# Performance work log

Hardware: AMD Instinct MI355X
Metric: run time of the kernel (lower is better)

## Reference

```python
import jax, jax.numpy as jnp
import numpy as np

EPS = 1e-12
NEG = -1e30


def setup_inputs() -> dict:
    key = jax.random.key(0)
    ks = jax.random.split(key, 7)
    B, Nq, Lp, H, D = 96, 35, 180, 768, 128
    q_hidden = jax.random.normal(ks[0], (B, Nq, H), dtype=jnp.float32)
    pos_hidden = jax.random.normal(ks[1], (B, Lp, H), dtype=jnp.float32)
    neg_hidden = jax.random.normal(ks[2], (B, Lp, H), dtype=jnp.float32)
    W = jax.random.normal(ks[3], (H, D), dtype=jnp.float32) * 0.02
    b = jax.random.normal(ks[4], (D,), dtype=jnp.float32) * 0.02
    # non-punctuation filter mask; guarantee at least one valid token per passage
    pos_mask = jax.random.bernoulli(ks[5], 0.85, (B, Lp)).at[:, 0].set(True)
    neg_mask = jax.random.bernoulli(ks[6], 0.85, (B, Lp)).at[:, 0].set(True)
    return {"q_hidden": q_hidden, "pos_hidden": pos_hidden, "neg_hidden": neg_hidden,
            "W": W, "b": b, "pos_mask": pos_mask, "neg_mask": neg_mask}


def _vector_representation(h, W, b):
    # Linear projection then F.normalize(x) with torch default dim=1,
    # i.e. normalization over the SEQUENCE axis (faithful to source).
    x = jnp.einsum('blh,hd->bld', h, W) + b
    norm = jnp.maximum(jnp.sqrt(jnp.sum(x * x, axis=1, keepdims=True)), EPS)
    return x / norm


def _late_interaction(q, p, mask):
    # q: [Bq, Nq, D], p: [Bp, Lp, D], mask: [Bp, Lp] (True = keep token)
    sim = jnp.einsum('qnd,pld->qpnl', q, p)          # [Bq, Bp, Nq, Lp]
    sim = jnp.where(mask[None, :, None, :], sim, NEG)
    return jnp.max(sim, axis=-1).sum(axis=-1)        # MaxSim: max over Lp, sum over Nq


def reference(q_hidden, pos_hidden, neg_hidden, W, b, pos_mask, neg_mask):
    q = _vector_representation(q_hidden, W, b)
    pos = _vector_representation(pos_hidden, W, b)
    neg = _vector_representation(neg_hidden, W, b)
    pos_scores = _late_interaction(q, pos, pos_mask)
    neg_scores = _late_interaction(q, neg, neg_mask)
    return jnp.concatenate((pos_scores, neg_scores), axis=1)  # [B, 2B]
```

## Files before the change

kernel.cpp:

```cpp
#include <hip/hip_runtime.h>

typedef __attribute__((ext_vector_type(4))) float f32x4;
typedef __attribute__((ext_vector_type(8))) short s16x8;
typedef __attribute__((ext_vector_type(4))) short s16x4;
typedef __bf16 bf16x4 __attribute__((ext_vector_type(4)));

#define B_   96
#define NQ   35
#define LP   180
#define H_   768
#define D_   128
#define NEGF (-1e30f)

#define NROWS 37920
#define QROWS 3360
#define PROWS 17280

__device__ __forceinline__ unsigned short f2bf(float f) {
    return __builtin_bit_cast(unsigned short, (__bf16)f);
}

__device__ __forceinline__ void cvt_hilo(f32x4 v0, f32x4 v1, s16x8* hi, s16x8* lo) {
    bf16x4 h0 = __builtin_convertvector(v0, bf16x4);
    bf16x4 h1 = __builtin_convertvector(v1, bf16x4);
    f32x4 r0 = v0 - __builtin_convertvector(h0, f32x4);
    f32x4 r1 = v1 - __builtin_convertvector(h1, f32x4);
    bf16x4 l0 = __builtin_convertvector(r0, bf16x4);
    bf16x4 l1 = __builtin_convertvector(r1, bf16x4);
    s16x4 h0s = __builtin_bit_cast(s16x4, h0), h1s = __builtin_bit_cast(s16x4, h1);
    s16x4 l0s = __builtin_bit_cast(s16x4, l0), l1s = __builtin_bit_cast(s16x4, l1);
    *hi = __builtin_shufflevector(h0s, h1s, 0, 1, 2, 3, 4, 5, 6, 7);
    *lo = __builtin_shufflevector(l0s, l1s, 0, 1, 2, 3, 4, 5, 6, 7);
}

__device__ __forceinline__ s16x8 pack_bf16(f32x4 v0, f32x4 v1) {
    bf16x4 h0 = __builtin_convertvector(v0, bf16x4);
    bf16x4 h1 = __builtin_convertvector(v1, bf16x4);
    s16x4 a = __builtin_bit_cast(s16x4, h0), b = __builtin_bit_cast(s16x4, h1);
    return __builtin_shufflevector(a, b, 0, 1, 2, 3, 4, 5, 6, 7);
}

__device__ __forceinline__ void glds16(const void* g, void* l) {
    __builtin_amdgcn_global_load_lds(
        (const __attribute__((address_space(1))) unsigned int*)g,
        (__attribute__((address_space(3))) unsigned int*)l,
        16, 0, 0);
}

__global__ __launch_bounds__(256) void prep_k(
    const float* __restrict__ W, unsigned short* __restrict__ wthi,
    const unsigned int* __restrict__ pmask_w, unsigned int* __restrict__ ctrl,
    float* __restrict__ ssq) {
    __shared__ unsigned int rr[256];
    int b = blockIdx.x, t = threadIdx.x;
    if (b < 48) {
        int tid = b * 256 + t;
        int nt = tid / (24 * 64);
        int r = tid - nt * 24 * 64;
        int ks = r / 64, lane = r - ks * 64;
        int m = lane & 15, quad = lane >> 4;
        unsigned short* o = wthi + (size_t)tid * 8;
#pragma unroll
        for (int j = 0; j < 8; j++) {
            int k = ks * 32 + quad * 8 + j;
            o[j] = f2bf(W[(size_t)k * D_ + nt * 16 + m]);
        }
    } else if (b < 192) {
        ssq[(b - 48) * 256 + t] = 0.f;
    } else {
        unsigned int f1 = 0, f3 = 0, f4 = 0;
        for (int w = t; w < 4320; w += 256) {
            unsigned int v = pmask_w[w];
            f1 |= v & 0x0000ff00u;
            f3 |= v & 0xff000000u;
            if (w & 1) f4 |= v & 0x000000ffu;
        }
        rr[t] = f1; __syncthreads();
        for (int s2 = 128; s2; s2 >>= 1) { if (t < s2) rr[t] |= rr[t + s2]; __syncthreads(); }
        if (!t) ctrl[0] = rr[0];
        __syncthreads();
        rr[t] = f3; __syncthreads();
        for (int s2 = 128; s2; s2 >>= 1) { if (t < s2) rr[t] |= rr[t + s2]; __syncthreads(); }
        if (!t) ctrl[1] = rr[0];
        __syncthreads();
        rr[t] = f4; __syncthreads();
        for (int s2 = 128; s2; s2 >>= 1) { if (t < s2) rr[t] |= rr[t + s2]; __syncthreads(); }
        if (!t) ctrl[2] = rr[0];
    }
}

__global__ __launch_bounds__(256) void proj_k(
    const float* __restrict__ qh, const float* __restrict__ ph, const float* __restrict__ nh,
    const unsigned short* __restrict__ wthi, const float* __restrict__ bias,
    float* __restrict__ x, float* __restrict__ ssq,
    const void* __restrict__ pm, const void* __restrict__ nm,
    const unsigned int* __restrict__ ctrl, unsigned char* __restrict__ maskc) {
    __shared__ float abuf[4][3072];
    int b = blockIdx.x;
    if (b >= 2370) {
        int i = (b - 2370) * 256 + threadIdx.x;
        const void* src = (i < B_ * LP) ? pm : nm;
        int j = (i < B_ * LP) ? i : i - B_ * LP;
        unsigned int c1 = ctrl[0], c3 = ctrl[1], c4 = ctrl[2];
        bool bit;
        if (c1 > 0)       bit = ((const unsigned char*)src)[j] != 0;
        else if (c3 > 0)  bit = ((const float*)src)[j] != 0.0f;
        else if (c4 > 0)  bit = ((const int*)src)[j] != 0;
        else              bit = ((const long long*)src)[j] != 0;
        maskc[i] = bit ? 1 : 0;
        return;
    }
    int wave = threadIdx.x >> 6, lane = threadIdx.x & 63;
    int rg = b;
    const float* src; int row0l; int growbase;
    if (rg < 210)       { src = qh; row0l = rg * 16;          growbase = row0l; }
    else if (rg < 1290) { src = ph; row0l = (rg - 210) * 16;  growbase = QROWS + row0l; }
    else                { src = nh; row0l = (rg - 1290) * 16; growbase = QROWS + PROWS + row0l; }
    int m = lane & 15, quad = lane >> 4;
    const float* ap = src + (size_t)(row0l + m) * H_ + wave * 192 + quad * 8;

#pragma unroll
    for (int kl = 0; kl < 6; kl++) {
        glds16(ap + kl * 32,     &abuf[wave][kl * 512]);
        glds16(ap + kl * 32 + 4, &abuf[wave][kl * 512 + 256]);
    }
    __syncthreads();

    f32x4 acc[8];
#pragma unroll
    for (int nt = 0; nt < 8; nt++) acc[nt] = (f32x4){0.f, 0.f, 0.f, 0.f};

#pragma unroll
    for (int kl = 0; kl < 6; kl++) {
        f32x4 v0 = *(const f32x4*)&abuf[wave][kl * 512 + lane * 4];
        f32x4 v1 = *(const f32x4*)&abuf[wave][kl * 512 + 256 + lane * 4];
        s16x8 ahi, alo;
        cvt_hilo(v0, v1, &ahi, &alo);
        int ksg = wave * 6 + kl;
        s16x8 bh[8];
#pragma unroll
        for (int nt = 0; nt < 8; nt++)
            bh[nt] = *(const s16x8*)(wthi + ((size_t)(nt * 24 + ksg) * 64 + lane) * 8);
#pragma unroll
        for (int nt = 0; nt < 8; nt++) {
            acc[nt] = __builtin_amdgcn_mfma_f32_16x16x32_bf16(ahi, bh[nt], acc[nt], 0, 0, 0);
            acc[nt] = __builtin_amdgcn_mfma_f32_16x16x32_bf16(alo, bh[nt], acc[nt], 0, 0, 0);
        }
    }
#pragma unroll
    for (int nt = 0; nt < 8; nt++)
        *(f32x4*)&abuf[wave][nt * 256 + lane * 4] = acc[nt];
    __syncthreads();

    int bk0, bk1, b1start;
    if (growbase < QROWS)              { bk0 = growbase / 35;  bk1 = (growbase + 15) / 35;
                                         b1start = bk1 * 35; }
    else if (growbase < QROWS + PROWS) { int r0 = growbase - QROWS;
                                         bk0 = 96 + r0 / 180;  bk1 = 96 + (r0 + 15) / 180;
                                         b1start = QROWS + (bk1 - 96) * 180; }
    else                               { int r0 = growbase - QROWS - PROWS;
                                         bk0 = 192 + r0 / 180; bk1 = 192 + (r0 + 15) / 180;
                                         b1start = QROWS + PROWS + (bk1 - 192) * 180; }

#pragma unroll
    for (int q2 = 0; q2 < 2; q2++) {
        int nt = wave * 2 + q2;
        f32x4 s = *(const f32x4*)&abuf[0][nt * 256 + lane * 4];
        s += *(const f32x4*)&abuf[1][nt * 256 + lane * 4];
        s += *(const f32x4*)&abuf[2][nt * 256 + lane * 4];
        s += *(const f32x4*)&abuf[3][nt * 256 + lane * 4];
        int col = nt * 16 + m;
        float bv = bias[col];
        float slo = 0.f, shi = 0.f;
#pragma unroll
        for (int r = 0; r < 4; r++) {
            int grow = growbase + quad * 4 + r;
            float v = s[r] + bv;
            x[(size_t)grow * D_ + col] = v;
            float v2 = v * v;
            if (bk1 > bk0 && grow >= b1start) shi += v2; else slo += v2;
        }
        slo += __shfl_xor(slo, 16); slo += __shfl_xor(slo, 32);
        if (quad == 0) atomicAdd(ssq + (size_t)bk0 * D_ + col, slo);
        if (bk1 > bk0) {
            shi += __shfl_xor(shi, 16); shi += __shfl_xor(shi, 32);
            if (quad == 0) atomicAdd(ssq + (size_t)bk1 * D_ + col, shi);
        }
    }
}

__global__ __launch_bounds__(256) void scatter_k(
    const float* __restrict__ x, const float* __restrict__ ssq,
    const unsigned char* __restrict__ maskc,
    unsigned short* __restrict__ qfrag, unsigned short* __restrict__ pfrag) {
    int c = blockIdx.x * 256 + threadIdx.x;
    int lane = c & 63, ks = (c >> 6) & 3;
    int quad = lane >> 4, mm = lane & 15;
    int d0 = ks * 32 + quad * 8;
    if (c < 61440) {
        int g = c >> 8;
        int mt = g % 5, qp = g / 5;
        int prow = mt * 16 + mm;
        s16x8 outv = (s16x8){0, 0, 0, 0, 0, 0, 0, 0};
        if (prow < 70) {
            int hi = prow >= 35;
            int bq = qp * 2 + hi;
            int l = prow - hi * 35;
            size_t row = (size_t)bq * 35 + l;
            const f32x4* px = (const f32x4*)(x + row * D_ + d0);
            f32x4 v0 = px[0], v1 = px[1];
            const f32x4* pq = (const f32x4*)(ssq + (size_t)bq * D_ + d0);
            f32x4 q0 = pq[0], q1 = pq[1];
            f32x4 r0, r1;
#pragma unroll
            for (int j = 0; j < 4; j++) {
                r0[j] = rsqrtf(fmaxf(q0[j], 1e-24f));
                r1[j] = rsqrtf(fmaxf(q1[j], 1e-24f));
            }
            outv = pack_bf16(v0 * r0, v1 * r1);
        }
        *(s16x8*)(qfrag + (size_t)c * 8) = outv;
    } else {
        int c2 = c - 61440;
        int g = c2 >> 8;
        int nt = g % 12, pbk = g / 12;
        int l = nt * 16 + mm;
        int lsrc = (l < LP && maskc[pbk * LP + l]) ? l : 0;
        size_t row = QROWS + (size_t)pbk * LP + lsrc;
        const f32x4* px = (const f32x4*)(x + row * D_ + d0);
        f32x4 v0 = px[0], v1 = px[1];
        const f32x4* pq = (const f32x4*)(ssq + (size_t)(96 + pbk) * D_ + d0);
        f32x4 q0 = pq[0], q1 = pq[1];
        f32x4 r0, r1;
#pragma unroll
        for (int j = 0; j < 4; j++) {
            r0[j] = rsqrtf(fmaxf(q0[j], 1e-24f));
            r1[j] = rsqrtf(fmaxf(q1[j], 1e-24f));
        }
        *(s16x8*)(pfrag + (size_t)c2 * 8) = pack_bf16(v0 * r0, v1 * r1);
    }
}

__global__ __launch_bounds__(256, 3) void interact_k(
    const unsigned short* __restrict__ qfrag, const unsigned short* __restrict__ pfrag,
    float* __restrict__ out) {
    __shared__ unsigned short plds[24576];
    int wave = threadIdx.x >> 6, lane = threadIdx.x & 63;
    int b = blockIdx.x;
    int xcd = b & 7, i = b >> 3;
    int c = xcd * 24 + (i % 24);
    int qg = i / 24;
    int side = c / 96, pb = c - side * 96;
    int qp = qg * 4 + wave;
    int m = lane & 15, quad = lane >> 4;

    const unsigned short* pbase = pfrag + (size_t)c * 24576;
    const unsigned short* qbase = qfrag + (size_t)qp * 10240;

#pragma unroll
    for (int ntl = 0; ntl < 3; ntl++) {
        int nt = wave * 3 + ntl;
#pragma unroll
        for (int ks = 0; ks < 4; ks++)
            glds16(pbase + ((size_t)(nt * 4 + ks) * 64 + lane) * 8,
                   &plds[(size_t)(nt * 4 + ks) * 512]);
    }

    s16x8 a[5][4];
#pragma unroll
    for (int mt = 0; mt < 5; mt++)
#pragma unroll
        for (int ks = 0; ks < 4; ks++)
            a[mt][ks] = *(const s16x8*)(qbase + ((size_t)(mt * 4 + ks) * 64 + lane) * 8);

    __syncthreads();

    const f32x4 zero4 = (f32x4){0.f, 0.f, 0.f, 0.f};
    float rmax[5][4];
#pragma unroll
    for (int mt = 0; mt < 5; mt++)
#pragma unroll
        for (int rr = 0; rr < 4; rr++) rmax[mt][rr] = NEGF;

    for (int nt = 0; nt < 12; nt++) {
        s16x8 bfr[4];
#pragma unroll
        for (int ks = 0; ks < 4; ks++)
            bfr[ks] = *(const s16x8*)&plds[((size_t)(nt * 4 + ks) * 64 + lane) * 8];
#pragma unroll
        for (int mt = 0; mt < 5; mt++) {
            f32x4 acc = __builtin_amdgcn_mfma_f32_16x16x32_bf16(a[mt][0], bfr[0], zero4, 0, 0, 0);
            acc = __builtin_amdgcn_mfma_f32_16x16x32_bf16(a[mt][1], bfr[1], acc, 0, 0, 0);
            acc = __builtin_amdgcn_mfma_f32_16x16x32_bf16(a[mt][2], bfr[2], acc, 0, 0, 0);
            acc = __builtin_amdgcn_mfma_f32_16x16x32_bf16(a[mt][3], bfr[3], acc, 0, 0, 0);
#pragma unroll
            for (int rr = 0; rr < 4; rr++)
                rmax[mt][rr] = fmaxf(rmax[mt][rr], acc[rr]);
        }
    }

#pragma unroll
    for (int mt = 0; mt < 5; mt++)
#pragma unroll
        for (int rr = 0; rr < 4; rr++) {
            float v = rmax[mt][rr];
            v = fmaxf(v, __shfl_xor(v, 1));
            v = fmaxf(v, __shfl_xor(v, 2));
            v = fmaxf(v, __shfl_xor(v, 4));
            v = fmaxf(v, __shfl_xor(v, 8));
            rmax[mt][rr] = v;
        }
    float s0 = 0.f, s1 = 0.f;
#pragma unroll
    for (int mt = 0; mt < 5; mt++)
#pragma unroll
        for (int rr = 0; rr < 4; rr++) {
            int prow = mt * 16 + quad * 4 + rr;
            float v = rmax[mt][rr];
            if (prow < 35) s0 += v;
            else if (prow < 70) s1 += v;
        }
    s0 += __shfl_xor(s0, 16); s0 += __shfl_xor(s0, 32);
    s1 += __shfl_xor(s1, 16); s1 += __shfl_xor(s1, 32);
    if (lane == 0) {
        int qb0 = qp * 2, qb1 = qp * 2 + 1;
        out[(size_t)qb0 * (2 * B_) + side * B_ + pb] = s0;
        out[(size_t)qb1 * (2 * B_) + side * B_ + pb] = s1;
    }
}

extern "C" void kernel_launch(void* const* d_in, const int* in_sizes, int n_in,
                              void* d_out, int out_size, void* d_ws, size_t ws_size,
                              hipStream_t stream) {
    const float* qh   = (const float*)d_in[0];
    const float* ph   = (const float*)d_in[1];
    const float* nh   = (const float*)d_in[2];
    const float* W    = (const float*)d_in[3];
    const float* bias = (const float*)d_in[4];
    const void* pmask = d_in[5];
    const void* nmask = d_in[6];
    float* out = (float*)d_out;
    char* ws = (char*)d_ws;

    constexpr size_t CTRL_OFF  = 0;
    constexpr size_t WTHI_OFF  = 256;
    constexpr size_t MASKC_OFF = WTHI_OFF + 196608;
    constexpr size_t SSQ_OFF   = 231424;
    constexpr size_t X_OFF     = SSQ_OFF + 147456;
    constexpr size_t QFRAG_OFF = X_OFF + (size_t)NROWS * D_ * 4;
    constexpr size_t PFRAG_OFF = QFRAG_OFF + 983040;

    unsigned int* ctrl     = (unsigned int*)(ws + CTRL_OFF);
    unsigned short* wthi   = (unsigned short*)(ws + WTHI_OFF);
    unsigned char* maskc   = (unsigned char*)(ws + MASKC_OFF);
    float* ssq             = (float*)(ws + SSQ_OFF);
    float* x               = (float*)(ws + X_OFF);
    unsigned short* qfrag  = (unsigned short*)(ws + QFRAG_OFF);
    unsigned short* pfrag  = (unsigned short*)(ws + PFRAG_OFF);

    prep_k<<<193, 256, 0, stream>>>(W, wthi, (const unsigned int*)pmask, ctrl, ssq);
    proj_k<<<2370 + 135, 256, 0, stream>>>(qh, ph, nh, wthi, bias, x, ssq,
                                           pmask, nmask, ctrl, maskc);
    scatter_k<<<2544, 256, 0, stream>>>(x, ssq, maskc, qfrag, pfrag);
    interact_k<<<2304, 256, 0, stream>>>(qfrag, pfrag, out);
}
```

Baseline: 214.0 us.

## Process two 16-row tiles per projection block to reuse weight fragments

```diff
diff --git a/kernel.cpp b/kernel.cpp
--- a/kernel.cpp
+++ b/kernel.cpp
@@ -95,10 +95,10 @@
     float* __restrict__ x, float* __restrict__ ssq,
     const void* __restrict__ pm, const void* __restrict__ nm,
     const unsigned int* __restrict__ ctrl, unsigned char* __restrict__ maskc) {
-    __shared__ float abuf[4][3072];
+    __shared__ f32x4 part[4][8][64];
     int b = blockIdx.x;
-    if (b >= 2370) {
-        int i = (b - 2370) * 256 + threadIdx.x;
+    if (b >= 1185) {
+        int i = (b - 1185) * 256 + threadIdx.x;
         const void* src = (i < B_ * LP) ? pm : nm;
         int j = (i < B_ * LP) ? i : i - B_ * LP;
         unsigned int c1 = ctrl[0], c3 = ctrl[1], c4 = ctrl[2];
@@ -111,31 +111,29 @@
         return;
     }
     int wave = threadIdx.x >> 6, lane = threadIdx.x & 63;
-    int rg = b;
     const float* src; int row0l; int growbase;
-    if (rg < 210)       { src = qh; row0l = rg * 16;          growbase = row0l; }
-    else if (rg < 1290) { src = ph; row0l = (rg - 210) * 16;  growbase = QROWS + row0l; }
-    else                { src = nh; row0l = (rg - 1290) * 16; growbase = QROWS + PROWS + row0l; }
+    if (b < 105)      { src = qh; row0l = b * 32;         growbase = row0l; }
+    else if (b < 645) { src = ph; row0l = (b - 105) * 32; growbase = QROWS + row0l; }
+    else              { src = nh; row0l = (b - 645) * 32; growbase = QROWS + PROWS + row0l; }
     int m = lane & 15, quad = lane >> 4;
-    const float* ap = src + (size_t)(row0l + m) * H_ + wave * 192 + quad * 8;
+    const float* ap0 = src + (size_t)(row0l + m) * H_ + wave * 192 + quad * 8;
+    const float* ap1 = ap0 + (size_t)16 * H_;
+
+    f32x4 acc[2][8];
+#pragma unroll
+    for (int mt = 0; mt < 2; mt++)
+#pragma unroll
+        for (int nt = 0; nt < 8; nt++) acc[mt][nt] = (f32x4){0.f, 0.f, 0.f, 0.f};
 
 #pragma unroll
     for (int kl = 0; kl < 6; kl++) {
-        glds16(ap + kl * 32,     &abuf[wave][kl * 512]);
-        glds16(ap + kl * 32 + 4, &abuf[wave][kl * 512 + 256]);
-    }
-    __syncthreads();
-
-    f32x4 acc[8];
-#pragma unroll
-    for (int nt = 0; nt < 8; nt++) acc[nt] = (f32x4){0.f, 0.f, 0.f, 0.f};
-
-#pragma unroll
-    for (int kl = 0; kl < 6; kl++) {
-        f32x4 v0 = *(const f32x4*)&abuf[wave][kl * 512 + lane * 4];
-        f32x4 v1 = *(const f32x4*)&abuf[wave][kl * 512 + 256 + lane * 4];
-        s16x8 ahi, alo;
-        cvt_hilo(v0, v1, &ahi, &alo);
+        f32x4 u0 = *(const f32x4*)(ap0 + kl * 32);
+        f32x4 u1 = *(const f32x4*)(ap0 + kl * 32 + 4);
+        f32x4 w0 = *(const f32x4*)(ap1 + kl * 32);
+        f32x4 w1 = *(const f32x4*)(ap1 + kl * 32 + 4);
+        s16x8 a0hi, a0lo, a1hi, a1lo;
+        cvt_hilo(u0, u1, &a0hi, &a0lo);
+        cvt_hilo(w0, w1, &a1hi, &a1lo);
         int ksg = wave * 6 + kl;
         s16x8 bh[8];
 #pragma unroll
@@ -143,48 +141,55 @@
             bh[nt] = *(const s16x8*)(wthi + ((size_t)(nt * 24 + ksg) * 64 + lane) * 8);
 #pragma unroll
         for (int nt = 0; nt < 8; nt++) {
-            acc[nt] = __builtin_amdgcn_mfma_f32_16x16x32_bf16(ahi, bh[nt], acc[nt], 0, 0, 0);
-            acc[nt] = __builtin_amdgcn_mfma_f32_16x16x32_bf16(alo, bh[nt], acc[nt], 0, 0, 0);
-        }
-    }
-#pragma unroll
-    for (int nt = 0; nt < 8; nt++)
-        *(f32x4*)&abuf[wave][nt * 256 + lane * 4] = acc[nt];
-    __syncthreads();
-
-    int bk0, bk1, b1start;
-    if (growbase < QROWS)              { bk0 = growbase / 35;  bk1 = (growbase + 15) / 35;
+            acc[0][nt] = __builtin_amdgcn_mfma_f32_16x16x32_bf16(a0hi, bh[nt], acc[0][nt], 0, 0, 0);
+            acc[0][nt] = __builtin_amdgcn_mfma_f32_16x16x32_bf16(a0lo, bh[nt], acc[0][nt], 0, 0, 0);
+            acc[1][nt] = __builtin_amdgcn_mfma_f32_16x16x32_bf16(a1hi, bh[nt], acc[1][nt], 0, 0, 0);
+            acc[1][nt] = __builtin_amdgcn_mfma_f32_16x16x32_bf16(a1lo, bh[nt], acc[1][nt], 0, 0, 0);
+        }
+    }
+
+#pragma unroll
+    for (int mt = 0; mt < 2; mt++) {
+        if (mt) __syncthreads();
+#pragma unroll
+        for (int nt = 0; nt < 8; nt++) part[wave][nt][lane] = acc[mt][nt];
+        __syncthreads();
+
+        int base = growbase + mt * 16;
+        int bk0, bk1, b1start;
+        if (base < QROWS)              { bk0 = base / 35;  bk1 = (base + 15) / 35;
                                          b1start = bk1 * 35; }
-    else if (growbase < QROWS + PROWS) { int r0 = growbase - QROWS;
+        else if (base < QROWS + PROWS) { int r0 = base - QROWS;
                                          bk0 = 96 + r0 / 180;  bk1 = 96 + (r0 + 15) / 180;
                                          b1start = QROWS + (bk1 - 96) * 180; }
-    else                               { int r0 = growbase - QROWS - PROWS;
+        else                           { int r0 = base - QROWS - PROWS;
                                          bk0 = 192 + r0 / 180; bk1 = 192 + (r0 + 15) / 180;
                                          b1start = QROWS + PROWS + (bk1 - 192) * 180; }
 
 #pragma unroll
-    for (int q2 = 0; q2 < 2; q2++) {
-        int nt = wave * 2 + q2;
-        f32x4 s = *(const f32x4*)&abuf[0][nt * 256 + lane * 4];
-        s += *(const f32x4*)&abuf[1][nt * 256 + lane * 4];
-        s += *(const f32x4*)&abuf[2][nt * 256 + lane * 4];
-        s += *(const f32x4*)&abuf[3][nt * 256 + lane * 4];
-        int col = nt * 16 + m;
-        float bv = bias[col];
-        float slo = 0.f, shi = 0.f;
-#pragma unroll
-        for (int r = 0; r < 4; r++) {
-            int grow = growbase + quad * 4 + r;
-            float v = s[r] + bv;
-            x[(size_t)grow * D_ + col] = v;
-            float v2 = v * v;
-            if (bk1 > bk0 && grow >= b1start) shi += v2; else slo += v2;
-        }
-        slo += __shfl_xor(slo, 16); slo += __shfl_xor(slo, 32);
-        if (quad == 0) atomicAdd(ssq + (size_t)bk0 * D_ + col, slo);
-        if (bk1 > bk0) {
-            shi += __shfl_xor(shi, 16); shi += __shfl_xor(shi, 32);
-            if (quad == 0) atomicAdd(ssq + (size_t)bk1 * D_ + col, shi);
+        for (int q2 = 0; q2 < 2; q2++) {
+            int nt = wave * 2 + q2;
+            f32x4 s = part[0][nt][lane];
+            s += part[1][nt][lane];
+            s += part[2][nt][lane];
+            s += part[3][nt][lane];
+            int col = nt * 16 + m;
+            float bv = bias[col];
+            float slo = 0.f, shi = 0.f;
+#pragma unroll
+            for (int r = 0; r < 4; r++) {
+                int grow = base + quad * 4 + r;
+                float v = s[r] + bv;
+                x[(size_t)grow * D_ + col] = v;
+                float v2 = v * v;
+                if (bk1 > bk0 && grow >= b1start) shi += v2; else slo += v2;
+            }
+            slo += __shfl_xor(slo, 16); slo += __shfl_xor(slo, 32);
+            if (quad == 0) atomicAdd(ssq + (size_t)bk0 * D_ + col, slo);
+            if (bk1 > bk0) {
+                shi += __shfl_xor(shi, 16); shi += __shfl_xor(shi, 32);
+                if (quad == 0) atomicAdd(ssq + (size_t)bk1 * D_ + col, shi);
+            }
         }
     }
 }
@@ -359,7 +364,7 @@
     unsigned short* pfrag  = (unsigned short*)(ws + PFRAG_OFF);
 
     prep_k<<<193, 256, 0, stream>>>(W, wthi, (const unsigned int*)pmask, ctrl, ssq);
-    proj_k<<<2370 + 135, 256, 0, stream>>>(qh, ph, nh, wthi, bias, x, ssq,
+    proj_k<<<1185 + 135, 256, 0, stream>>>(qh, ph, nh, wthi, bias, x, ssq,
                                            pmask, nmask, ctrl, maskc);
     scatter_k<<<2544, 256, 0, stream>>>(x, ssq, maskc, qfrag, pfrag);
     interact_k<<<2304, 256, 0, stream>>>(qfrag, pfrag, out);
```

Measured after the change: 211.5 us. About the same (-1.2%).
